# Kernel tuning notes

Hardware: AMD Instinct MI355X
Metric: run time of the kernel (lower is better)

Reference implementation:

```python
import jax, jax.numpy as jnp
import numpy as np

D_MODEL = 256; N_HEADS = 8; HEAD_DIM = 32; N_LEVELS = 4; N_POINTS = 4; N_LAYERS = 3; D_FFN = 1024
SHAPES = np.array([[76, 76], [38, 38], [19, 19], [10, 10]], dtype=np.int64)
S_TOTAL = int((SHAPES[:, 0] * SHAPES[:, 1]).sum())  # 7681


def setup_inputs():
    key = jax.random.key(0)
    ks = jax.random.split(key, 12)
    B = 1; C = D_MODEL; M = N_HEADS; Lv = N_LEVELS; P = N_POINTS; L = N_LAYERS; s = 0.02
    starts = np.concatenate([[0], np.cumsum(SHAPES[:, 0] * SHAPES[:, 1])[:-1]]).astype(np.int64)
    inp = {
        "src": jax.random.normal(ks[0], (B, S_TOTAL, C), jnp.float32),
        "pos": jax.random.normal(ks[1], (B, S_TOTAL, C), jnp.float32),
        "valid_ratios": jnp.ones((B, Lv, 2), jnp.float32),
        "spatial_shapes": jnp.asarray(SHAPES),
        "level_start_index": jnp.asarray(starts),
        "padding_mask": jnp.zeros((B, S_TOTAL), bool),
        "W_off": jax.random.normal(ks[2], (L, C, M * Lv * P * 2), jnp.float32) * s,
        "b_off": jax.random.normal(ks[3], (L, M * Lv * P * 2), jnp.float32) * s,
        "W_attn": jax.random.normal(ks[4], (L, C, M * Lv * P), jnp.float32) * s,
        "b_attn": jax.random.normal(ks[5], (L, M * Lv * P), jnp.float32) * s,
        "W_val": jax.random.normal(ks[6], (L, C, C), jnp.float32) * s,
        "b_val": jnp.zeros((L, C), jnp.float32),
        "W_out": jax.random.normal(ks[7], (L, C, C), jnp.float32) * s,
        "b_out": jnp.zeros((L, C), jnp.float32),
        "ln1_g": jnp.ones((L, C), jnp.float32),
        "ln1_b": jnp.zeros((L, C), jnp.float32),
        "W_ff1": jax.random.normal(ks[8], (L, C, D_FFN), jnp.float32) * s,
        "b_ff1": jnp.zeros((L, D_FFN), jnp.float32),
        "W_ff2": jax.random.normal(ks[9], (L, D_FFN, C), jnp.float32) * s,
        "b_ff2": jnp.zeros((L, C), jnp.float32),
        "ln2_g": jnp.ones((L, C), jnp.float32),
        "ln2_b": jnp.zeros((L, C), jnp.float32),
    }
    return inp


def _ln(x, g, b):
    mu = x.mean(-1, keepdims=True)
    var = ((x - mu) ** 2).mean(-1, keepdims=True)
    return (x - mu) * jax.lax.rsqrt(var + 1e-5) * g + b


def _gather(v, idx):
    # v: [B, HW, M, D], idx: [B, S, M, P] -> [B, S, M, P, D], head-specific gather
    B, S, M, P = idx.shape
    def one(vb, ib):
        i2 = ib.transpose(0, 2, 1).reshape(S * P, M, 1)
        o = jnp.take_along_axis(vb, i2, axis=0)  # [S*P, M, D]
        return o.reshape(S, P, M, -1).transpose(0, 2, 1, 3)
    return jax.vmap(one)(v, idx)


def _msda(query, src, mask, ref, shapes, starts, Wo, bo, Wa, ba, Wv, bv, Wout, bout):
    # Multi-scale deformable attention (Deformable-DETR), grid_sample align_corners=False + zero padding
    B, S, C = src.shape
    M, Lv, P, D = N_HEADS, N_LEVELS, N_POINTS, HEAD_DIM
    value = src @ Wv + bv
    value = jnp.where(mask[..., None], 0.0, value).reshape(B, S, M, D)
    off = (query @ Wo + bo).reshape(B, S, M, Lv, P, 2)
    aw = jax.nn.softmax((query @ Wa + ba).reshape(B, S, M, Lv * P), -1).reshape(B, S, M, Lv, P)
    norm = jnp.asarray(shapes[:, ::-1].copy(), jnp.float32)  # (W, H) per level
    loc = ref[:, :, None, :, None, :] + off / norm[None, None, None, :, None, :]  # [B,S,M,Lv,P,2]
    out = jnp.zeros((B, S, M, D), query.dtype)
    for lvl in range(Lv):
        H = int(shapes[lvl, 0]); W = int(shapes[lvl, 1]); st = int(starts[lvl])
        v = value[:, st:st + H * W]  # [B, H*W, M, D]
        l = loc[:, :, :, lvl]  # [B, S, M, P, 2]
        x = l[..., 0] * W - 0.5
        y = l[..., 1] * H - 0.5
        x0 = jnp.floor(x); y0 = jnp.floor(y)
        dx = x - x0; dy = y - y0
        samp = jnp.zeros((B, S, M, P, D), query.dtype)
        for yy, xx, w in ((y0, x0, (1 - dy) * (1 - dx)), (y0, x0 + 1, (1 - dy) * dx),
                          (y0 + 1, x0, dy * (1 - dx)), (y0 + 1, x0 + 1, dy * dx)):
            valid = (xx >= 0) & (xx < W) & (yy >= 0) & (yy < H)
            xi = jnp.clip(xx, 0, W - 1).astype(jnp.int32)
            yi = jnp.clip(yy, 0, H - 1).astype(jnp.int32)
            g = _gather(v, yi * W + xi)
            samp = samp + (w * valid)[..., None] * g
        out = out + (aw[:, :, :, lvl, :, None] * samp).sum(3)
    return out.reshape(B, S, C) @ Wout + bout


def _ref_points(vr, shapes):
    refs = []
    for lvl in range(shapes.shape[0]):
        H = int(shapes[lvl, 0]); W = int(shapes[lvl, 1])
        ry, rx = np.meshgrid(np.linspace(0.5, H - 0.5, H, dtype=np.float32),
                             np.linspace(0.5, W - 0.5, W, dtype=np.float32), indexing="ij")
        rxj = jnp.asarray(rx.reshape(-1))[None] / (vr[:, None, lvl, 0] * W)
        ryj = jnp.asarray(ry.reshape(-1))[None] / (vr[:, None, lvl, 1] * H)
        refs.append(jnp.stack([rxj, ryj], -1))
    ref = jnp.concatenate(refs, 1)  # [B, S, 2]
    return ref[:, :, None] * vr[:, None]  # [B, S, Lv, 2]


def _encoder(src, pos, valid_ratios, shapes, starts, mask, params):
    (W_off, b_off, W_attn, b_attn, W_val, b_val, W_out, b_out,
     ln1_g, ln1_b, W_ff1, b_ff1, W_ff2, b_ff2, ln2_g, ln2_b) = params
    ref = _ref_points(valid_ratios, shapes)
    out = src
    for l in range(N_LAYERS):
        q = out + pos  # with_pos_embed
        a = _msda(q, out, mask, ref, shapes, starts, W_off[l], b_off[l], W_attn[l], b_attn[l],
                  W_val[l], b_val[l], W_out[l], b_out[l])
        out = _ln(out + a, ln1_g[l], ln1_b[l])
        f = jax.nn.relu(out @ W_ff1[l] + b_ff1[l]) @ W_ff2[l] + b_ff2[l]
        out = _ln(out + f, ln2_g[l], ln2_b[l])
    return out


def reference(src, pos, valid_ratios, spatial_shapes, level_start_index, padding_mask,
              W_off, b_off, W_attn, b_attn, W_val, b_val, W_out, b_out,
              ln1_g, ln1_b, W_ff1, b_ff1, W_ff2, b_ff2, ln2_g, ln2_b):
    shapes = np.asarray(spatial_shapes)
    starts = np.asarray(level_start_index)
    params = (W_off, b_off, W_attn, b_attn, W_val, b_val, W_out, b_out,
              ln1_g, ln1_b, W_ff1, b_ff1, W_ff2, b_ff2, ln2_g, ln2_b)
    return _encoder(src, pos, valid_ratios, shapes, starts, padding_mask, params)
```

## Files before the change

kernel.cpp:

```cpp
#include <hip/hip_runtime.h>
#include <hip/hip_bf16.h>
#include <math.h>

#define S_TOTAL 7681

typedef __attribute__((ext_vector_type(8))) short bf16x8;
typedef __attribute__((ext_vector_type(4))) float f32x4;

__device__ __forceinline__ short f2b(float x) {
    union { float f; unsigned u; } v; v.f = x;
    unsigned r = v.u + 0x7FFFu + ((v.u >> 16) & 1u);
    return (short)(r >> 16);
}
__device__ __forceinline__ float b2f(unsigned short u) {
    union { unsigned u; float f; } t; t.u = ((unsigned)u) << 16; return t.f;
}

__global__ __launch_bounds__(256) void transpose_cvt_kernel(
    const float* __restrict__ s0, const float* __restrict__ s1,
    const float* __restrict__ s2, const float* __restrict__ s3,
    const float* __restrict__ s4, const float* __restrict__ s5,
    short* __restrict__ d0, short* __restrict__ d1, short* __restrict__ d2,
    short* __restrict__ d3, short* __restrict__ d4, short* __restrict__ d5)
{
    const int z = blockIdx.z;
    int t = blockIdx.x;
    const float* src; short* dst; int K, N, lt;
    if (t < 64)       { src = s0 + (size_t)z * 65536;  dst = d0 + (size_t)z * 65536;  K = 256;  N = 256;  lt = t; }
    else if (t < 128) { src = s1 + (size_t)z * 65536;  dst = d1 + (size_t)z * 98304;  K = 256;  N = 256;  lt = t - 64; }
    else if (t < 160) { src = s2 + (size_t)z * 32768;  dst = d2 + (size_t)z * 98304;  K = 256;  N = 128;  lt = t - 128; }
    else if (t < 224) { src = s3 + (size_t)z * 65536;  dst = d3 + (size_t)z * 65536;  K = 256;  N = 256;  lt = t - 160; }
    else if (t < 480) { src = s4 + (size_t)z * 262144; dst = d4 + (size_t)z * 262144; K = 256;  N = 1024; lt = t - 224; }
    else              { src = s5 + (size_t)z * 262144; dst = d5 + (size_t)z * 262144; K = 1024; N = 256;  lt = t - 480; }
    const int ntx = N >> 5;
    const int tk = (lt / ntx) << 5, tn = (lt % ntx) << 5;
    __shared__ float tile[32][33];
    const int cx = threadIdx.x & 31, cy = threadIdx.x >> 5;
    #pragma unroll
    for (int i = 0; i < 32; i += 8)
        tile[cy + i][cx] = src[(size_t)(tk + cy + i) * N + tn + cx];
    __syncthreads();
    #pragma unroll
    for (int i = 0; i < 32; i += 8)
        dst[(size_t)(tn + cy + i) * K + tk + cx] = f2b(tile[cx][cy + i]);
}

#define BM 128
#define BN 64
#define BK 64
#define KP 72

__global__ __launch_bounds__(256) void gemm_va_kernel(
    const short* __restrict__ xb, const short* __restrict__ qb,
    const short* __restrict__ Wt_val, const short* __restrict__ Wt_oa,
    const float* __restrict__ b_val, const float* __restrict__ b_off,
    const float* __restrict__ b_attn,
    short* __restrict__ value_bf, float* __restrict__ offbuf, int M)
{
    const int grp = (blockIdx.y >= 4);
    const short* A  = grp ? qb : xb;
    const short* Wt = grp ? Wt_oa : Wt_val;
    const int colBase = (grp ? (blockIdx.y - 4) : blockIdx.y) * BN;
    const int K = 256;

    __shared__ __align__(16) short As[BM * KP];
    __shared__ __align__(16) short Bs[BN * KP];
    const int tid = threadIdx.x;
    const int lane = tid & 63;
    const int wave = tid >> 6;
    const int rowBase = blockIdx.x * BM;

    const int ar = tid >> 1;
    const int ak = (tid & 1) * 32;
    const int br = tid >> 2;
    const int bk = (tid & 3) * 16;

    const int frow = lane & 15;
    const int fko  = (lane >> 4) * 8;
    const int wm = wave * 32;

    f32x4 acc[2][4] = {};

    const int aRow = rowBase + ar;
    const bool aOk = aRow < M;
    const short* Ap = A + (size_t)aRow * K + ak;
    const short* Bp = Wt + (size_t)(colBase + br) * K + bk;

    bf16x8 a0 = {}, a1 = {}, a2 = {}, a3 = {}, b0 = {}, b1 = {};
    if (aOk) {
        a0 = *(const bf16x8*)Ap;        a1 = *(const bf16x8*)(Ap + 8);
        a2 = *(const bf16x8*)(Ap + 16); a3 = *(const bf16x8*)(Ap + 24);
    }
    b0 = *(const bf16x8*)Bp; b1 = *(const bf16x8*)(Bp + 8);

    for (int k0 = 0; k0 < K; k0 += BK) {
        *(bf16x8*)&As[ar * KP + ak]      = a0;
        *(bf16x8*)&As[ar * KP + ak + 8]  = a1;
        *(bf16x8*)&As[ar * KP + ak + 16] = a2;
        *(bf16x8*)&As[ar * KP + ak + 24] = a3;
        *(bf16x8*)&Bs[br * KP + bk]      = b0;
        *(bf16x8*)&Bs[br * KP + bk + 8]  = b1;
        __syncthreads();

        const int kn = k0 + BK;
        if (kn < K) {
            if (aOk) {
                a0 = *(const bf16x8*)(Ap + kn);      a1 = *(const bf16x8*)(Ap + kn + 8);
                a2 = *(const bf16x8*)(Ap + kn + 16); a3 = *(const bf16x8*)(Ap + kn + 24);
            }
            b0 = *(const bf16x8*)(Bp + kn); b1 = *(const bf16x8*)(Bp + kn + 8);
        }

        #pragma unroll
        for (int kk = 0; kk < BK; kk += 32) {
            bf16x8 af0 = *(const bf16x8*)&As[(wm + frow) * KP + kk + fko];
            bf16x8 af1 = *(const bf16x8*)&As[(wm + 16 + frow) * KP + kk + fko];
            #pragma unroll
            for (int j = 0; j < 4; ++j) {
                bf16x8 bfj = *(const bf16x8*)&Bs[(j * 16 + frow) * KP + kk + fko];
                acc[0][j] = __builtin_amdgcn_mfma_f32_16x16x32_bf16(af0, bfj, acc[0][j], 0, 0, 0);
                acc[1][j] = __builtin_amdgcn_mfma_f32_16x16x32_bf16(af1, bfj, acc[1][j], 0, 0, 0);
            }
        }
        __syncthreads();
    }

    const int erow = (lane >> 4) * 4;
    const int ecol = lane & 15;
    #pragma unroll
    for (int mi = 0; mi < 2; ++mi) {
        #pragma unroll
        for (int j = 0; j < 4; ++j) {
            int col = colBase + j * 16 + ecol;
            float bias = grp ? (col < 256 ? b_off[col] : b_attn[col - 256]) : b_val[col];
            #pragma unroll
            for (int r = 0; r < 4; ++r) {
                int row = rowBase + wm + mi * 16 + erow + r;
                if (row < M) {
                    float v = acc[mi][j][r] + bias;
                    if (grp) offbuf[(size_t)row * 384 + col] = v;
                    else     value_bf[(size_t)row * 256 + col] = f2b(v);
                }
            }
        }
    }
}

template<int RELU, int OUTBF>
__global__ __launch_bounds__(256) void gemm_kernel(
    const short* __restrict__ A, const short* __restrict__ Wt,
    const float* __restrict__ bias, void* __restrict__ Cv,
    int M, int N, int K)
{
    __shared__ __align__(16) short As[BM * KP];
    __shared__ __align__(16) short Bs[BN * KP];
    const int tid = threadIdx.x;
    const int lane = tid & 63;
    const int wave = tid >> 6;
    const int rowBase = blockIdx.x * BM;
    const int colBase = blockIdx.y * BN;

    const int ar = tid >> 1;
    const int ak = (tid & 1) * 32;
    const int br = tid >> 2;
    const int bk = (tid & 3) * 16;

    const int frow = lane & 15;
    const int fko  = (lane >> 4) * 8;
    const int wm = wave * 32;

    f32x4 acc[2][4] = {};

    const int aRow = rowBase + ar;
    const bool aOk = aRow < M;
    const short* Ap = A + (size_t)aRow * K + ak;
    const short* Bp = Wt + (size_t)(colBase + br) * K + bk;

    bf16x8 a0 = {}, a1 = {}, a2 = {}, a3 = {}, b0 = {}, b1 = {};
    if (aOk) {
        a0 = *(const bf16x8*)Ap;        a1 = *(const bf16x8*)(Ap + 8);
        a2 = *(const bf16x8*)(Ap + 16); a3 = *(const bf16x8*)(Ap + 24);
    }
    b0 = *(const bf16x8*)Bp; b1 = *(const bf16x8*)(Bp + 8);

    for (int k0 = 0; k0 < K; k0 += BK) {
        *(bf16x8*)&As[ar * KP + ak]      = a0;
        *(bf16x8*)&As[ar * KP + ak + 8]  = a1;
        *(bf16x8*)&As[ar * KP + ak + 16] = a2;
        *(bf16x8*)&As[ar * KP + ak + 24] = a3;
        *(bf16x8*)&Bs[br * KP + bk]      = b0;
        *(bf16x8*)&Bs[br * KP + bk + 8]  = b1;
        __syncthreads();

        const int kn = k0 + BK;
        if (kn < K) {
            if (aOk) {
                a0 = *(const bf16x8*)(Ap + kn);      a1 = *(const bf16x8*)(Ap + kn + 8);
                a2 = *(const bf16x8*)(Ap + kn + 16); a3 = *(const bf16x8*)(Ap + kn + 24);
            }
            b0 = *(const bf16x8*)(Bp + kn); b1 = *(const bf16x8*)(Bp + kn + 8);
        }

        #pragma unroll
        for (int kk = 0; kk < BK; kk += 32) {
            bf16x8 af0 = *(const bf16x8*)&As[(wm + frow) * KP + kk + fko];
            bf16x8 af1 = *(const bf16x8*)&As[(wm + 16 + frow) * KP + kk + fko];
            #pragma unroll
            for (int j = 0; j < 4; ++j) {
                bf16x8 bfj = *(const bf16x8*)&Bs[(j * 16 + frow) * KP + kk + fko];
                acc[0][j] = __builtin_amdgcn_mfma_f32_16x16x32_bf16(af0, bfj, acc[0][j], 0, 0, 0);
                acc[1][j] = __builtin_amdgcn_mfma_f32_16x16x32_bf16(af1, bfj, acc[1][j], 0, 0, 0);
            }
        }
        __syncthreads();
    }

    const int erow = (lane >> 4) * 4;
    const int ecol = lane & 15;
    #pragma unroll
    for (int mi = 0; mi < 2; ++mi) {
        #pragma unroll
        for (int j = 0; j < 4; ++j) {
            #pragma unroll
            for (int r = 0; r < 4; ++r) {
                int row = rowBase + wm + mi * 16 + erow + r;
                if (row < M) {
                    int col = colBase + j * 16 + ecol;
                    float v = acc[mi][j][r] + bias[col];
                    if (RELU) v = fmaxf(v, 0.f);
                    if (OUTBF) ((short*)Cv)[(size_t)row * N + col] = f2b(v);
                    else       ((float*)Cv)[(size_t)row * N + col] = v;
                }
            }
        }
    }
}

template<int WRITEQ>
__global__ __launch_bounds__(256) void gemm_ln_kernel(
    const short* __restrict__ A, const short* __restrict__ Wt,
    const float* __restrict__ bias, const float* __restrict__ g,
    const float* __restrict__ bln, const float* __restrict__ pos,
    float* __restrict__ out, short* __restrict__ xb, short* __restrict__ qb,
    int M, int K)
{
    __shared__ __align__(16) short As[16 * KP];
    __shared__ __align__(16) short Bs[256 * KP];
    __shared__ float rsum[16][4], rsq[16][4], smu[16], srs[16];

    const int tid = threadIdx.x;
    const int lane = tid & 63;
    const int wave = tid >> 6;
    const int rowBase = blockIdx.x * 16;

    const int frow = lane & 15;
    const int fko  = (lane >> 4) * 8;

    f32x4 acc[4] = {};

    const int ar = tid >> 3;
    const int ac = (tid & 7) * 8;
    const int aRow = rowBase + ar;
    const bool aOk = (tid < 128) && (aRow < M);
    const short* Ap = A + (size_t)aRow * K + ac;
    const short* Bp = Wt + (size_t)tid * K;

    bf16x8 a0 = {};
    bf16x8 w[8];
    if (aOk) a0 = *(const bf16x8*)Ap;
    #pragma unroll
    for (int i = 0; i < 8; ++i) w[i] = *(const bf16x8*)(Bp + i * 8);

    for (int k0 = 0; k0 < K; k0 += BK) {
        if (tid < 128) *(bf16x8*)&As[ar * KP + ac] = a0;
        #pragma unroll
        for (int i = 0; i < 8; ++i) *(bf16x8*)&Bs[tid * KP + i * 8] = w[i];
        __syncthreads();

        const int kn = k0 + BK;
        if (kn < K) {
            if (aOk) a0 = *(const bf16x8*)(Ap + kn);
            #pragma unroll
            for (int i = 0; i < 8; ++i) w[i] = *(const bf16x8*)(Bp + kn + i * 8);
        }

        #pragma unroll
        for (int kk = 0; kk < BK; kk += 32) {
            bf16x8 af = *(const bf16x8*)&As[frow * KP + kk + fko];
            #pragma unroll
            for (int j = 0; j < 4; ++j) {
                bf16x8 bfj = *(const bf16x8*)&Bs[(wave * 64 + j * 16 + frow) * KP + kk + fko];
                acc[j] = __builtin_amdgcn_mfma_f32_16x16x32_bf16(af, bfj, acc[j], 0, 0, 0);
            }
        }
        __syncthreads();
    }

    const int erow = (lane >> 4) * 4;
    const int ecol = lane & 15;
    float x[4][4];
    #pragma unroll
    for (int j = 0; j < 4; ++j)
        #pragma unroll
        for (int r = 0; r < 4; ++r) {
            int row = rowBase + erow + r;
            int col = wave * 64 + j * 16 + ecol;
            float res = (row < M) ? out[(size_t)row * 256 + col] : 0.f;
            x[j][r] = acc[j][r] + bias[col] + res;
        }

    #pragma unroll
    for (int r = 0; r < 4; ++r) {
        float s1 = x[0][r] + x[1][r] + x[2][r] + x[3][r];
        float s2 = x[0][r]*x[0][r] + x[1][r]*x[1][r]
                 + x[2][r]*x[2][r] + x[3][r]*x[3][r];
        #pragma unroll
        for (int o = 1; o < 16; o <<= 1) {
            s1 += __shfl_xor(s1, o);
            s2 += __shfl_xor(s2, o);
        }
        if ((lane & 15) == 0) {
            rsum[erow + r][wave] = s1;
            rsq [erow + r][wave] = s2;
        }
    }
    __syncthreads();
    if (tid < 16) {
        float S1 = rsum[tid][0] + rsum[tid][1] + rsum[tid][2] + rsum[tid][3];
        float S2 = rsq[tid][0] + rsq[tid][1] + rsq[tid][2] + rsq[tid][3];
        float mu = S1 * (1.f / 256.f);
        smu[tid] = mu;
        srs[tid] = rsqrtf(S2 * (1.f / 256.f) - mu * mu + 1e-5f);
    }
    __syncthreads();

    #pragma unroll
    for (int r = 0; r < 4; ++r) {
        int lrow = erow + r;
        int row = rowBase + lrow;
        if (row >= M) continue;
        float mu = smu[lrow], rs = srs[lrow];
        #pragma unroll
        for (int j = 0; j < 4; ++j) {
            int col = wave * 64 + j * 16 + ecol;
            float y = (x[j][r] - mu) * rs * g[col] + bln[col];
            out[(size_t)row * 256 + col] = y;
            xb[(size_t)row * 256 + col] = f2b(y);
            if (WRITEQ)
                qb[(size_t)row * 256 + col] = f2b(y + pos[(size_t)row * 256 + col]);
        }
    }
}

__global__ __launch_bounds__(256) void msda_kernel(
    const short* __restrict__ value, const float* __restrict__ offb,
    short* __restrict__ msdab)
{
    __shared__ float   soff[8 * 384];
    __shared__ ushort4 sIdx[1024];
    __shared__ float4  sWgt[1024];

    const int bid = blockIdx.x;
    const int sb = (bid & 7) * 121 + (bid >> 3);
    const int q0 = sb * 8;
    if (q0 >= S_TOTAL) return;
    const int tid = threadIdx.x;

    {
        const float4* src4 = (const float4*)offb;
        #pragma unroll
        for (int i = tid; i < 768; i += 256) {
            int qi = i / 96, j = i - qi * 96;
            int q = min(q0 + qi, S_TOTAL - 1);
            *(float4*)&soff[qi * 384 + j * 4] = src4[(size_t)q * 96 + j];
        }
    }
    __syncthreads();

    if (tid < 64) {
        const int qi = tid >> 3, m = tid & 7;
        float* lg = &soff[qi * 384 + 256 + m * 16];
        float mx = -1e30f;
        #pragma unroll
        for (int k = 0; k < 16; ++k) mx = fmaxf(mx, lg[k]);
        float e[16], sum = 0.f;
        #pragma unroll
        for (int k = 0; k < 16; ++k) { e[k] = expf(lg[k] - mx); sum += e[k]; }
        float inv = 1.f / sum;
        #pragma unroll
        for (int k = 0; k < 16; ++k) lg[k] = e[k] * inv;
    }
    __syncthreads();

    #pragma unroll
    for (int it = tid; it < 1024; it += 256) {
        const int qi = it >> 7, i = it & 127;
        const int lvl = (i >> 2) & 3;
        const int q = min(q0 + qi, S_TOTAL - 1);

        float refx, refy;
        if (q < 5776)      { int t = q;        int r = t / 76, c = t % 76; refx = (c + 0.5f) / 76.f; refy = (r + 0.5f) / 76.f; }
        else if (q < 7220) { int t = q - 5776; int r = t / 38, c = t % 38; refx = (c + 0.5f) / 38.f; refy = (r + 0.5f) / 38.f; }
        else if (q < 7581) { int t = q - 7220; int r = t / 19, c = t % 19; refx = (c + 0.5f) / 19.f; refy = (r + 0.5f) / 19.f; }
        else               { int t = q - 7581; int r = t / 10, c = t % 10; refx = (c + 0.5f) / 10.f; refy = (r + 0.5f) / 10.f; }

        const int LVL_HW[4] = {76, 38, 19, 10};
        const int LVL_ST[4] = {0, 5776, 7220, 7581};
        const int W = LVL_HW[lvl];
        const float fW = (float)W;

        float ox = soff[qi * 384 + i * 2];
        float oy = soff[qi * 384 + i * 2 + 1];
        float aw = soff[qi * 384 + 256 + i];

        float x = refx * fW + ox - 0.5f;
        float y = refy * fW + oy - 0.5f;
        float x0f = floorf(x), y0f = floorf(y);
        int x0 = (int)x0f, y0 = (int)y0f;
        float dx = x - x0f, dy = y - y0f;

        bool vx0 = (x0 >= 0) & (x0 < W);
        bool vx1 = (x0 >= -1) & (x0 < W - 1);
        bool vy0 = (y0 >= 0) & (y0 < W);
        bool vy1 = (y0 >= -1) & (y0 < W - 1);
        int xc0 = min(max(x0, 0), W - 1), xc1 = min(max(x0 + 1, 0), W - 1);
        int yc0 = min(max(y0, 0), W - 1), yc1 = min(max(y0 + 1, 0), W - 1);
        int base = LVL_ST[lvl];
        ushort4 id;
        id.x = (unsigned short)(base + yc0 * W + xc0);
        id.y = (unsigned short)(base + yc0 * W + xc1);
        id.z = (unsigned short)(base + yc1 * W + xc0);
        id.w = (unsigned short)(base + yc1 * W + xc1);
        float4 w4;
        w4.x = (vy0 && vx0) ? (1.f - dy) * (1.f - dx) * aw : 0.f;
        w4.y = (vy0 && vx1) ? (1.f - dy) * dx * aw : 0.f;
        w4.z = (vy1 && vx0) ? dy * (1.f - dx) * aw : 0.f;
        w4.w = (vy1 && vx1) ? dy * dx * aw : 0.f;
        sIdx[it] = id;
        sWgt[it] = w4;
    }
    __syncthreads();

    const int lane = tid & 63;
    const int qi = (tid >> 6) * 2 + (lane >> 5);
    const int q = q0 + qi;
    if (q >= S_TOTAL) return;
    const int l32 = lane & 31;
    const int h = l32 >> 2, dg = l32 & 3;
    const short* vcol = value + h * 32 + dg * 8;
    const int itb = qi * 128 + (h << 4);

    float a[8] = {};
    #pragma unroll
    for (int pt = 0; pt < 16; ++pt) {
        const ushort4 id = sIdx[itb + pt];
        const float4 w = sWgt[itb + pt];
        bf16x8 v0 = *(const bf16x8*)(vcol + ((size_t)id.x << 8));
        bf16x8 v1 = *(const bf16x8*)(vcol + ((size_t)id.y << 8));
        bf16x8 v2 = *(const bf16x8*)(vcol + ((size_t)id.z << 8));
        bf16x8 v3 = *(const bf16x8*)(vcol + ((size_t)id.w << 8));
        #pragma unroll
        for (int e = 0; e < 8; ++e)
            a[e] += w.x * b2f((unsigned short)v0[e]) + w.y * b2f((unsigned short)v1[e])
                  + w.z * b2f((unsigned short)v2[e]) + w.w * b2f((unsigned short)v3[e]);
    }
    bf16x8 o;
    #pragma unroll
    for (int e = 0; e < 8; ++e) o[e] = f2b(a[e]);
    *(bf16x8*)(msdab + (size_t)q * 256 + h * 32 + dg * 8) = o;
}

__global__ __launch_bounds__(256) void cvt_copy_kernel(
    const float4* __restrict__ src, const float4* __restrict__ pos,
    float4* __restrict__ o, ushort4* __restrict__ xb, ushort4* __restrict__ qb,
    int n4)
{
    int i = blockIdx.x * blockDim.x + threadIdx.x;
    if (i < n4) {
        float4 v = src[i], p = pos[i];
        o[i] = v;
        ushort4 h, hq;
        h.x = (unsigned short)f2b(v.x); h.y = (unsigned short)f2b(v.y);
        h.z = (unsigned short)f2b(v.z); h.w = (unsigned short)f2b(v.w);
        hq.x = (unsigned short)f2b(v.x + p.x); hq.y = (unsigned short)f2b(v.y + p.y);
        hq.z = (unsigned short)f2b(v.z + p.z); hq.w = (unsigned short)f2b(v.w + p.w);
        xb[i] = h;
        qb[i] = hq;
    }
}

extern "C" void kernel_launch(void* const* d_in, const int* in_sizes, int n_in,
                              void* d_out, int out_size, void* d_ws, size_t ws_size,
                              hipStream_t stream) {
    const float* src    = (const float*)d_in[0];
    const float* pos    = (const float*)d_in[1];
    const float* W_off  = (const float*)d_in[6];
    const float* b_off  = (const float*)d_in[7];
    const float* W_attn = (const float*)d_in[8];
    const float* b_attn = (const float*)d_in[9];
    const float* W_val  = (const float*)d_in[10];
    const float* b_val  = (const float*)d_in[11];
    const float* W_out  = (const float*)d_in[12];
    const float* b_out  = (const float*)d_in[13];
    const float* ln1_g  = (const float*)d_in[14];
    const float* ln1_b  = (const float*)d_in[15];
    const float* W_ff1  = (const float*)d_in[16];
    const float* b_ff1  = (const float*)d_in[17];
    const float* W_ff2  = (const float*)d_in[18];
    const float* b_ff2  = (const float*)d_in[19];
    const float* ln2_g  = (const float*)d_in[20];
    const float* ln2_b  = (const float*)d_in[21];

    const size_t S = S_TOTAL;
    float* out = (float*)d_out;

    short* wt = (short*)d_ws;
    short* Wt_val = wt;
    short* Wt_oa  = wt + 196608;
    short* Wt_out = wt + 491520;
    short* Wt_ff1 = wt + 688128;
    short* Wt_ff2 = wt + 1474560;
    float* fbase  = (float*)d_ws + 1131648;
    short* xb       = (short*)fbase;
    short* qb       = (short*)(fbase + 128 * S);
    short* value_bf = (short*)(fbase + 256 * S);
    float* offb     = fbase + 384 * S;
    short* msdab    = (short*)(fbase + 768 * S);
    short* hid      = (short*)(fbase + 256 * S);

    transpose_cvt_kernel<<<dim3(736, 1, 3), 256, 0, stream>>>(
        W_val, W_off, W_attn, W_out, W_ff1, W_ff2,
        Wt_val, Wt_oa, Wt_oa + 65536, Wt_out, Wt_ff1, Wt_ff2);

    const int n4 = (int)(S * 256 / 4);
    const int g4 = (n4 + 255) / 256;
    cvt_copy_kernel<<<g4, 256, 0, stream>>>((const float4*)src, (const float4*)pos,
                                            (float4*)out, (ushort4*)xb, (ushort4*)qb, n4);

    const int MB = (S_TOTAL + BM - 1) / BM;
    const int LB = (S_TOTAL + 15) / 16;

    for (int l = 0; l < 3; ++l) {
        gemm_va_kernel<<<dim3(MB, 10), 256, 0, stream>>>(
            xb, qb, Wt_val + (size_t)l * 65536, Wt_oa + (size_t)l * 98304,
            b_val + (size_t)l * 256, b_off + (size_t)l * 256, b_attn + (size_t)l * 128,
            value_bf, offb, S_TOTAL);
        msda_kernel<<<968, 256, 0, stream>>>(value_bf, offb, msdab);
        gemm_ln_kernel<0><<<LB, 256, 0, stream>>>(
            msdab, Wt_out + (size_t)l * 65536, b_out + (size_t)l * 256,
            ln1_g + (size_t)l * 256, ln1_b + (size_t)l * 256, pos,
            out, xb, qb, S_TOTAL, 256);
        gemm_kernel<1, 1><<<dim3(MB, 16), 256, 0, stream>>>(
            xb, Wt_ff1 + (size_t)l * 262144, b_ff1 + (size_t)l * 1024, hid,
            S_TOTAL, 1024, 256);
        gemm_ln_kernel<1><<<LB, 256, 0, stream>>>(
            hid, Wt_ff2 + (size_t)l * 262144, b_ff2 + (size_t)l * 256,
            ln2_g + (size_t)l * 256, ln2_b + (size_t)l * 256, pos,
            out, xb, qb, S_TOTAL, 1024);
    }
}
```

Before: 420.2 us.

## Drop LDS staging in GEMMs; load MFMA fragments directly from global memory

Rewrites all three GEMM kernels (value/offset projection, FFN1, and the GEMM+LayerNorm kernels) so each wave loads its MFMA A and B fragments straight from global memory into registers, with one-step register prefetch. This removes the shared-memory tiles and the __syncthreads barriers. Out-of-range rows are clamped instead of zero-filled. The cost is that data is no longer shared across waves through LDS, so global and L2 traffic goes up, and the fragment loads are strided 16-byte reads per lane rather than coalesced tile loads.

```diff
diff --git a/kernel.cpp b/kernel.cpp
--- a/kernel.cpp
+++ b/kernel.cpp
@@ -45,10 +45,8 @@
         dst[(size_t)(tn + cy + i) * K + tk + cx] = f2b(tile[cx][cy + i]);
 }
 
-#define BM 128
-#define BN 64
-#define BK 64
-#define KP 72
+
+#define MFMA16(a, b, c) __builtin_amdgcn_mfma_f32_16x16x32_bf16(a, b, c, 0, 0, 0)
 
 __global__ __launch_bounds__(256) void gemm_va_kernel(
     const short* __restrict__ xb, const short* __restrict__ qb,
@@ -60,69 +58,45 @@
     const int grp = (blockIdx.y >= 4);
     const short* A  = grp ? qb : xb;
     const short* Wt = grp ? Wt_oa : Wt_val;
-    const int colBase = (grp ? (blockIdx.y - 4) : blockIdx.y) * BN;
+    const int colBase = (grp ? (blockIdx.y - 4) : blockIdx.y) * 64;
     const int K = 256;
 
-    __shared__ __align__(16) short As[BM * KP];
-    __shared__ __align__(16) short Bs[BN * KP];
     const int tid = threadIdx.x;
     const int lane = tid & 63;
     const int wave = tid >> 6;
-    const int rowBase = blockIdx.x * BM;
-
-    const int ar = tid >> 1;
-    const int ak = (tid & 1) * 32;
-    const int br = tid >> 2;
-    const int bk = (tid & 3) * 16;
+    const int rowBase = blockIdx.x * 128 + wave * 32;
 
     const int frow = lane & 15;
-    const int fko  = (lane >> 4) * 8;
-    const int wm = wave * 32;
+    const int fk   = (lane >> 4) * 8;
+
+    const int r0 = min(rowBase + frow, M - 1);
+    const int r1 = min(rowBase + 16 + frow, M - 1);
+    const short* Ap0 = A + (size_t)r0 * K + fk;
+    const short* Ap1 = A + (size_t)r1 * K + fk;
+    const short* Bp0 = Wt + (size_t)(colBase +      frow) * K + fk;
+    const short* Bp1 = Wt + (size_t)(colBase + 16 + frow) * K + fk;
+    const short* Bp2 = Wt + (size_t)(colBase + 32 + frow) * K + fk;
+    const short* Bp3 = Wt + (size_t)(colBase + 48 + frow) * K + fk;
 
     f32x4 acc[2][4] = {};
 
-    const int aRow = rowBase + ar;
-    const bool aOk = aRow < M;
-    const short* Ap = A + (size_t)aRow * K + ak;
-    const short* Bp = Wt + (size_t)(colBase + br) * K + bk;
-
-    bf16x8 a0 = {}, a1 = {}, a2 = {}, a3 = {}, b0 = {}, b1 = {};
-    if (aOk) {
-        a0 = *(const bf16x8*)Ap;        a1 = *(const bf16x8*)(Ap + 8);
-        a2 = *(const bf16x8*)(Ap + 16); a3 = *(const bf16x8*)(Ap + 24);
-    }
-    b0 = *(const bf16x8*)Bp; b1 = *(const bf16x8*)(Bp + 8);
-
-    for (int k0 = 0; k0 < K; k0 += BK) {
-        *(bf16x8*)&As[ar * KP + ak]      = a0;
-        *(bf16x8*)&As[ar * KP + ak + 8]  = a1;
-        *(bf16x8*)&As[ar * KP + ak + 16] = a2;
-        *(bf16x8*)&As[ar * KP + ak + 24] = a3;
-        *(bf16x8*)&Bs[br * KP + bk]      = b0;
-        *(bf16x8*)&Bs[br * KP + bk + 8]  = b1;
-        __syncthreads();
-
-        const int kn = k0 + BK;
+    bf16x8 a0 = *(const bf16x8*)Ap0, a1 = *(const bf16x8*)Ap1;
+    bf16x8 b0 = *(const bf16x8*)Bp0, b1 = *(const bf16x8*)Bp1;
+    bf16x8 b2 = *(const bf16x8*)Bp2, b3 = *(const bf16x8*)Bp3;
+
+    #pragma unroll
+    for (int k = 0; k < K; k += 32) {
+        bf16x8 ca0 = a0, ca1 = a1, cb0 = b0, cb1 = b1, cb2 = b2, cb3 = b3;
+        const int kn = k + 32;
         if (kn < K) {
-            if (aOk) {
-                a0 = *(const bf16x8*)(Ap + kn);      a1 = *(const bf16x8*)(Ap + kn + 8);
-                a2 = *(const bf16x8*)(Ap + kn + 16); a3 = *(const bf16x8*)(Ap + kn + 24);
-            }
-            b0 = *(const bf16x8*)(Bp + kn); b1 = *(const bf16x8*)(Bp + kn + 8);
-        }
-
-        #pragma unroll
-        for (int kk = 0; kk < BK; kk += 32) {
-            bf16x8 af0 = *(const bf16x8*)&As[(wm + frow) * KP + kk + fko];
-            bf16x8 af1 = *(const bf16x8*)&As[(wm + 16 + frow) * KP + kk + fko];
-            #pragma unroll
-            for (int j = 0; j < 4; ++j) {
-                bf16x8 bfj = *(const bf16x8*)&Bs[(j * 16 + frow) * KP + kk + fko];
-                acc[0][j] = __builtin_amdgcn_mfma_f32_16x16x32_bf16(af0, bfj, acc[0][j], 0, 0, 0);
-                acc[1][j] = __builtin_amdgcn_mfma_f32_16x16x32_bf16(af1, bfj, acc[1][j], 0, 0, 0);
-            }
-        }
-        __syncthreads();
+            a0 = *(const bf16x8*)(Ap0 + kn); a1 = *(const bf16x8*)(Ap1 + kn);
+            b0 = *(const bf16x8*)(Bp0 + kn); b1 = *(const bf16x8*)(Bp1 + kn);
+            b2 = *(const bf16x8*)(Bp2 + kn); b3 = *(const bf16x8*)(Bp3 + kn);
+        }
+        acc[0][0] = MFMA16(ca0, cb0, acc[0][0]); acc[1][0] = MFMA16(ca1, cb0, acc[1][0]);
+        acc[0][1] = MFMA16(ca0, cb1, acc[0][1]); acc[1][1] = MFMA16(ca1, cb1, acc[1][1]);
+        acc[0][2] = MFMA16(ca0, cb2, acc[0][2]); acc[1][2] = MFMA16(ca1, cb2, acc[1][2]);
+        acc[0][3] = MFMA16(ca0, cb3, acc[0][3]); acc[1][3] = MFMA16(ca1, cb3, acc[1][3]);
     }
 
     const int erow = (lane >> 4) * 4;
@@ -135,7 +109,7 @@
             float bias = grp ? (col < 256 ? b_off[col] : b_attn[col - 256]) : b_val[col];
             #pragma unroll
             for (int r = 0; r < 4; ++r) {
-                int row = rowBase + wm + mi * 16 + erow + r;
+                int row = rowBase + mi * 16 + erow + r;
                 if (row < M) {
                     float v = acc[mi][j][r] + bias;
                     if (grp) offbuf[(size_t)row * 384 + col] = v;
@@ -152,67 +126,42 @@
     const float* __restrict__ bias, void* __restrict__ Cv,
     int M, int N, int K)
 {
-    __shared__ __align__(16) short As[BM * KP];
-    __shared__ __align__(16) short Bs[BN * KP];
     const int tid = threadIdx.x;
     const int lane = tid & 63;
     const int wave = tid >> 6;
-    const int rowBase = blockIdx.x * BM;
-    const int colBase = blockIdx.y * BN;
-
-    const int ar = tid >> 1;
-    const int ak = (tid & 1) * 32;
-    const int br = tid >> 2;
-    const int bk = (tid & 3) * 16;
+    const int rowBase = blockIdx.x * 128 + wave * 32;
+    const int colBase = blockIdx.y * 64;
 
     const int frow = lane & 15;
-    const int fko  = (lane >> 4) * 8;
-    const int wm = wave * 32;
+    const int fk   = (lane >> 4) * 8;
+
+    const int r0 = min(rowBase + frow, M - 1);
+    const int r1 = min(rowBase + 16 + frow, M - 1);
+    const short* Ap0 = A + (size_t)r0 * K + fk;
+    const short* Ap1 = A + (size_t)r1 * K + fk;
+    const short* Bp0 = Wt + (size_t)(colBase +      frow) * K + fk;
+    const short* Bp1 = Wt + (size_t)(colBase + 16 + frow) * K + fk;
+    const short* Bp2 = Wt + (size_t)(colBase + 32 + frow) * K + fk;
+    const short* Bp3 = Wt + (size_t)(colBase + 48 + frow) * K + fk;
 
     f32x4 acc[2][4] = {};
 
-    const int aRow = rowBase + ar;
-    const bool aOk = aRow < M;
-    const short* Ap = A + (size_t)aRow * K + ak;
-    const short* Bp = Wt + (size_t)(colBase + br) * K + bk;
-
-    bf16x8 a0 = {}, a1 = {}, a2 = {}, a3 = {}, b0 = {}, b1 = {};
-    if (aOk) {
-        a0 = *(const bf16x8*)Ap;        a1 = *(const bf16x8*)(Ap + 8);
-        a2 = *(const bf16x8*)(Ap + 16); a3 = *(const bf16x8*)(Ap + 24);
-    }
-    b0 = *(const bf16x8*)Bp; b1 = *(const bf16x8*)(Bp + 8);
-
-    for (int k0 = 0; k0 < K; k0 += BK) {
-        *(bf16x8*)&As[ar * KP + ak]      = a0;
-        *(bf16x8*)&As[ar * KP + ak + 8]  = a1;
-        *(bf16x8*)&As[ar * KP + ak + 16] = a2;
-        *(bf16x8*)&As[ar * KP + ak + 24] = a3;
-        *(bf16x8*)&Bs[br * KP + bk]      = b0;
-        *(bf16x8*)&Bs[br * KP + bk + 8]  = b1;
-        __syncthreads();
-
-        const int kn = k0 + BK;
+    bf16x8 a0 = *(const bf16x8*)Ap0, a1 = *(const bf16x8*)Ap1;
+    bf16x8 b0 = *(const bf16x8*)Bp0, b1 = *(const bf16x8*)Bp1;
+    bf16x8 b2 = *(const bf16x8*)Bp2, b3 = *(const bf16x8*)Bp3;
+
+    for (int k = 0; k < K; k += 32) {
+        bf16x8 ca0 = a0, ca1 = a1, cb0 = b0, cb1 = b1, cb2 = b2, cb3 = b3;
+        const int kn = k + 32;
         if (kn < K) {
-            if (aOk) {
-                a0 = *(const bf16x8*)(Ap + kn);      a1 = *(const bf16x8*)(Ap + kn + 8);
-                a2 = *(const bf16x8*)(Ap + kn + 16); a3 = *(const bf16x8*)(Ap + kn + 24);
-            }
-            b0 = *(const bf16x8*)(Bp + kn); b1 = *(const bf16x8*)(Bp + kn + 8);
-        }
-
-        #pragma unroll
-        for (int kk = 0; kk < BK; kk += 32) {
-            bf16x8 af0 = *(const bf16x8*)&As[(wm + frow) * KP + kk + fko];
-            bf16x8 af1 = *(const bf16x8*)&As[(wm + 16 + frow) * KP + kk + fko];
-            #pragma unroll
-            for (int j = 0; j < 4; ++j) {
-                bf16x8 bfj = *(const bf16x8*)&Bs[(j * 16 + frow) * KP + kk + fko];
-                acc[0][j] = __builtin_amdgcn_mfma_f32_16x16x32_bf16(af0, bfj, acc[0][j], 0, 0, 0);
-                acc[1][j] = __builtin_amdgcn_mfma_f32_16x16x32_bf16(af1, bfj, acc[1][j], 0, 0, 0);
-            }
-        }
-        __syncthreads();
+            a0 = *(const bf16x8*)(Ap0 + kn); a1 = *(const bf16x8*)(Ap1 + kn);
+            b0 = *(const bf16x8*)(Bp0 + kn); b1 = *(const bf16x8*)(Bp1 + kn);
+            b2 = *(const bf16x8*)(Bp2 + kn); b3 = *(const bf16x8*)(Bp3 + kn);
+        }
+        acc[0][0] = MFMA16(ca0, cb0, acc[0][0]); acc[1][0] = MFMA16(ca1, cb0, acc[1][0]);
+        acc[0][1] = MFMA16(ca0, cb1, acc[0][1]); acc[1][1] = MFMA16(ca1, cb1, acc[1][1]);
+        acc[0][2] = MFMA16(ca0, cb2, acc[0][2]); acc[1][2] = MFMA16(ca1, cb2, acc[1][2]);
+        acc[0][3] = MFMA16(ca0, cb3, acc[0][3]); acc[1][3] = MFMA16(ca1, cb3, acc[1][3]);
     }
 
     const int erow = (lane >> 4) * 4;
@@ -223,7 +172,7 @@
         for (int j = 0; j < 4; ++j) {
             #pragma unroll
             for (int r = 0; r < 4; ++r) {
-                int row = rowBase + wm + mi * 16 + erow + r;
+                int row = rowBase + mi * 16 + erow + r;
                 if (row < M) {
                     int col = colBase + j * 16 + ecol;
                     float v = acc[mi][j][r] + bias[col];
@@ -244,8 +193,6 @@
     float* __restrict__ out, short* __restrict__ xb, short* __restrict__ qb,
     int M, int K)
 {
-    __shared__ __align__(16) short As[16 * KP];
-    __shared__ __align__(16) short Bs[256 * KP];
     __shared__ float rsum[16][4], rsq[16][4], smu[16], srs[16];
 
     const int tid = threadIdx.x;
@@ -254,46 +201,35 @@
     const int rowBase = blockIdx.x * 16;
 
     const int frow = lane & 15;
-    const int fko  = (lane >> 4) * 8;
+    const int fk   = (lane >> 4) * 8;
+
+    const int r0 = min(rowBase + frow, M - 1);
+    const short* Ap  = A + (size_t)r0 * K + fk;
+    const int cb = wave * 64;
+    const short* Bp0 = Wt + (size_t)(cb +      frow) * K + fk;
+    const short* Bp1 = Wt + (size_t)(cb + 16 + frow) * K + fk;
+    const short* Bp2 = Wt + (size_t)(cb + 32 + frow) * K + fk;
+    const short* Bp3 = Wt + (size_t)(cb + 48 + frow) * K + fk;
 
     f32x4 acc[4] = {};
 
-    const int ar = tid >> 3;
-    const int ac = (tid & 7) * 8;
-    const int aRow = rowBase + ar;
-    const bool aOk = (tid < 128) && (aRow < M);
-    const short* Ap = A + (size_t)aRow * K + ac;
-    const short* Bp = Wt + (size_t)tid * K;
-
-    bf16x8 a0 = {};
-    bf16x8 w[8];
-    if (aOk) a0 = *(const bf16x8*)Ap;
-    #pragma unroll
-    for (int i = 0; i < 8; ++i) w[i] = *(const bf16x8*)(Bp + i * 8);
-
-    for (int k0 = 0; k0 < K; k0 += BK) {
-        if (tid < 128) *(bf16x8*)&As[ar * KP + ac] = a0;
-        #pragma unroll
-        for (int i = 0; i < 8; ++i) *(bf16x8*)&Bs[tid * KP + i * 8] = w[i];
-        __syncthreads();
-
-        const int kn = k0 + BK;
+    bf16x8 a0 = *(const bf16x8*)Ap;
+    bf16x8 b0 = *(const bf16x8*)Bp0, b1 = *(const bf16x8*)Bp1;
+    bf16x8 b2 = *(const bf16x8*)Bp2, b3 = *(const bf16x8*)Bp3;
+
+    #pragma unroll 4
+    for (int k = 0; k < K; k += 32) {
+        bf16x8 ca = a0, cb0 = b0, cb1 = b1, cb2 = b2, cb3 = b3;
+        const int kn = k + 32;
         if (kn < K) {
-            if (aOk) a0 = *(const bf16x8*)(Ap + kn);
-            #pragma unroll
-            for (int i = 0; i < 8; ++i) w[i] = *(const bf16x8*)(Bp + kn + i * 8);
-        }
-
-        #pragma unroll
-        for (int kk = 0; kk < BK; kk += 32) {
-            bf16x8 af = *(const bf16x8*)&As[frow * KP + kk + fko];
-            #pragma unroll
-            for (int j = 0; j < 4; ++j) {
-                bf16x8 bfj = *(const bf16x8*)&Bs[(wave * 64 + j * 16 + frow) * KP + kk + fko];
-                acc[j] = __builtin_amdgcn_mfma_f32_16x16x32_bf16(af, bfj, acc[j], 0, 0, 0);
-            }
-        }
-        __syncthreads();
+            a0 = *(const bf16x8*)(Ap + kn);
+            b0 = *(const bf16x8*)(Bp0 + kn); b1 = *(const bf16x8*)(Bp1 + kn);
+            b2 = *(const bf16x8*)(Bp2 + kn); b3 = *(const bf16x8*)(Bp3 + kn);
+        }
+        acc[0] = MFMA16(ca, cb0, acc[0]);
+        acc[1] = MFMA16(ca, cb1, acc[1]);
+        acc[2] = MFMA16(ca, cb2, acc[2]);
+        acc[3] = MFMA16(ca, cb3, acc[3]);
     }
 
     const int erow = (lane >> 4) * 4;
@@ -304,7 +240,7 @@
         #pragma unroll
         for (int r = 0; r < 4; ++r) {
             int row = rowBase + erow + r;
-            int col = wave * 64 + j * 16 + ecol;
+            int col = cb + j * 16 + ecol;
             float res = (row < M) ? out[(size_t)row * 256 + col] : 0.f;
             x[j][r] = acc[j][r] + bias[col] + res;
         }
@@ -342,7 +278,7 @@
         float mu = smu[lrow], rs = srs[lrow];
         #pragma unroll
         for (int j = 0; j < 4; ++j) {
-            int col = wave * 64 + j * 16 + ecol;
+            int col = cb + j * 16 + ecol;
             float y = (x[j][r] - mu) * rs * g[col] + bln[col];
             out[(size_t)row * 256 + col] = y;
             xb[(size_t)row * 256 + col] = f2b(y);
@@ -537,7 +473,7 @@
     cvt_copy_kernel<<<g4, 256, 0, stream>>>((const float4*)src, (const float4*)pos,
                                             (float4*)out, (ushort4*)xb, (ushort4*)qb, n4);
 
-    const int MB = (S_TOTAL + BM - 1) / BM;
+    const int MB = (S_TOTAL + 127) / 128;
     const int LB = (S_TOTAL + 15) / 16;
 
     for (int l = 0; l < 3; ++l) {
```

Result: slower. 504.4 us (+20.0%).
